# Optimization experiments

Measured on AMD Instinct MI355X. Metric: run time of the kernel, lower is better.

The kernel has to match this reference:

```python
import jax, jax.numpy as jnp
import numpy as np

N_NODES = 50000
N_EDGES = 500000
NEG_SLOPE = 0.2


def gat_layer(x, src, dst, W, a_src, a_dst, b, n):
    """PyG-style GATConv (add_self_loops=True, concat=True, eval mode).
    x: [N, F_in], W: [F_in, H*C], a_src/a_dst: [H, C], b: [H*C]."""
    H, C = a_src.shape
    h = (x @ W).reshape(-1, H, C)              # [N, H, C]
    loops = jnp.arange(n, dtype=src.dtype)
    s = jnp.concatenate([src, loops])          # self-loops appended
    d = jnp.concatenate([dst, loops])
    alpha_src = jnp.einsum('nhc,hc->nh', h, a_src)   # [N, H]
    alpha_dst = jnp.einsum('nhc,hc->nh', h, a_dst)
    e = jax.nn.leaky_relu(alpha_src[s] + alpha_dst[d], NEG_SLOPE)  # [E+N, H]
    m = jax.ops.segment_max(e, d, num_segments=n)    # segment softmax over dst
    w = jnp.exp(e - m[d])
    denom = jax.ops.segment_sum(w, d, num_segments=n)
    attn = w / (denom[d] + 1e-16)                    # [E+N, H]
    msg = h[s] * attn[:, :, None]                    # [E+N, H, C]
    out = jax.ops.segment_sum(msg, d, num_segments=n)  # [N, H, C]
    return out.reshape(n, H * C) + b


def setup_inputs() -> dict:
    key = jax.random.key(0)
    ks = jax.random.split(key, 20)
    F_in, Hd, Hh = 128, 64, 4
    g = lambda k, shp, fan: jax.random.normal(k, shp, jnp.float32) * (1.0 / np.sqrt(fan))
    inp = {
        'x': jax.random.normal(ks[0], (N_NODES, F_in), jnp.float32),
        'edge_index': jax.random.randint(ks[1], (2, N_EDGES), 0, N_NODES, jnp.int32),
        'W1': g(ks[2], (F_in, Hh * Hd), F_in),
        'a1s': g(ks[3], (Hh, Hd), Hd), 'a1d': g(ks[4], (Hh, Hd), Hd),
        'b1': jnp.zeros((Hh * Hd,), jnp.float32),
        'W2': g(ks[5], (Hh * Hd, Hh * Hd), Hh * Hd),
        'a2s': g(ks[6], (Hh, Hd), Hd), 'a2d': g(ks[7], (Hh, Hd), Hd),
        'b2': jnp.zeros((Hh * Hd,), jnp.float32),
        'W3': g(ks[8], (Hh * Hd, Hd), Hh * Hd),
        'a3s': g(ks[9], (1, Hd), Hd), 'a3d': g(ks[10], (1, Hd), Hd),
        'b3': jnp.zeros((Hd,), jnp.float32),
        'cW1': g(ks[11], (Hd, Hd // 2), Hd), 'cb1': jnp.zeros((Hd // 2,), jnp.float32),
        'cW2': g(ks[12], (Hd // 2, 2), Hd // 2), 'cb2': jnp.zeros((2,), jnp.float32),
    }
    return inp


def reference(x, edge_index, W1, a1s, a1d, b1, W2, a2s, a2d, b2,
              W3, a3s, a3d, b3, cW1, cb1, cW2, cb2):
    n = x.shape[0]
    src, dst = edge_index[0], edge_index[1]
    h = jax.nn.elu(gat_layer(x, src, dst, W1, a1s, a1d, b1, n))
    h = jax.nn.elu(gat_layer(h, src, dst, W2, a2s, a2d, b2, n))
    h = jax.nn.relu(gat_layer(h, src, dst, W3, a3s, a3d, b3, n))
    h = jax.nn.relu(h @ cW1 + cb1)
    logits = h @ cW2 + cb2
    return jax.nn.log_softmax(logits, axis=1)
```

## Files before the change

### kernel.cpp

```cpp
#include <hip/hip_runtime.h>
#include <hip/hip_fp16.h>

#define LRELU(v) ((v) > 0.f ? (v) : 0.2f * (v))
#define LOG2E 1.44269504088896340736f

typedef _Float16 f16x8 __attribute__((ext_vector_type(8)));
typedef _Float16 f16x4 __attribute__((ext_vector_type(4)));
typedef float f32x4 __attribute__((ext_vector_type(4)));

__device__ __forceinline__ float fexp2(float x) {
    return __builtin_amdgcn_exp2f(x);
}

__device__ __forceinline__ f16x8 f16x8_zero() {
    f16x8 v;
#pragma unroll
    for (int j = 0; j < 8; ++j) v[j] = (_Float16)0.f;
    return v;
}

__global__ __launch_bounds__(256) void hist_kernel(const int* __restrict__ dst,
                                                   int* __restrict__ cnt, int E) {
    int e = blockIdx.x * 256 + threadIdx.x;
    if (e < E) atomicAdd(&cnt[dst[e]], 1);
}

__global__ __launch_bounds__(256) void scan_blk(const int* __restrict__ cnt,
                                                int* __restrict__ offv,
                                                int* __restrict__ bsum, int N) {
    __shared__ int sh[256];
    const int t = threadIdx.x;
    const int base = blockIdx.x * 1024 + t * 4;
    int v0 = (base + 0 < N) ? cnt[base + 0] : 0;
    int v1 = (base + 1 < N) ? cnt[base + 1] : 0;
    int v2 = (base + 2 < N) ? cnt[base + 2] : 0;
    int v3 = (base + 3 < N) ? cnt[base + 3] : 0;
    const int T = v0 + v1 + v2 + v3;
    sh[t] = T;
    __syncthreads();
    for (int o = 1; o < 256; o <<= 1) {
        int x = (t >= o) ? sh[t - o] : 0;
        __syncthreads();
        sh[t] += x;
        __syncthreads();
    }
    const int excl = sh[t] - T;
    if (t == 255) bsum[blockIdx.x] = sh[255];
    if (base + 0 < N) offv[base + 0] = excl;
    if (base + 1 < N) offv[base + 1] = excl + v0;
    if (base + 2 < N) offv[base + 2] = excl + v0 + v1;
    if (base + 3 < N) offv[base + 3] = excl + v0 + v1 + v2;
}

__global__ __launch_bounds__(64) void scan_top(int* __restrict__ bsum,
                                               int* __restrict__ offv,
                                               int NB, int N) {
    const int t = threadIdx.x;
    const int v = (t < NB) ? bsum[t] : 0;
    int incl = v;
#pragma unroll
    for (int o = 1; o < 64; o <<= 1) {
        int x = __shfl_up(incl, o);
        if (t >= o) incl += x;
    }
    if (t < NB) bsum[t] = incl - v;
    if (t == NB - 1) offv[N] = incl;
}

__global__ __launch_bounds__(256) void scan_add(int* __restrict__ offv,
                                                const int* __restrict__ bsum, int N) {
    const int base = blockIdx.x * 1024 + threadIdx.x * 4;
    const int add = bsum[blockIdx.x];
#pragma unroll
    for (int i = 0; i < 4; ++i)
        if (base + i < N) offv[base + i] += add;
}

__global__ __launch_bounds__(256) void fill_kernel(const int* __restrict__ dst,
                                                   const int* __restrict__ srcv,
                                                   const int* __restrict__ offv,
                                                   int* __restrict__ cur,
                                                   int* __restrict__ csrsrc, int E) {
    int e = blockIdx.x * 256 + threadIdx.x;
    if (e < E) {
        int d = dst[e];
        int p = atomicAdd(&cur[d], 1);
        csrsrc[offv[d] + p] = srcv[e];
    }
}

__global__ __launch_bounds__(256) void prep_w_all(
    const float* __restrict__ W1, const float* __restrict__ W2,
    const float* __restrict__ W3, _Float16* __restrict__ Wt1,
    _Float16* __restrict__ Wt2, _Float16* __restrict__ Wt3) {
    const int S1 = 128 * 256, S2 = 256 * 256, S3 = 256 * 64;
    int idx = blockIdx.x * 256 + threadIdx.x;
    if (idx < S1) {
        int k = idx >> 8, nn = idx & 255;
        Wt1[nn * 128 + k] = (_Float16)W1[idx];
    } else if (idx < S1 + S2) {
        int i = idx - S1;
        int k = i >> 8, nn = i & 255;
        Wt2[nn * 256 + k] = (_Float16)W2[idx - S1];
    } else if (idx < S1 + S2 + S3) {
        int i = idx - S1 - S2;
        int k = i >> 6, nn = i & 63;
        Wt3[nn * 256 + k] = (_Float16)W3[i];
    }
}

template <int WM, int WN, int K, int H, bool AF32>
__global__ __launch_bounds__(WM * WN * 64) void gemm_f16_fused(
    const void* __restrict__ Av, const _Float16* __restrict__ Wt,
    const float* __restrict__ a_s, const float* __restrict__ a_d,
    _Float16* __restrict__ hout, float* __restrict__ als,
    float* __restrict__ ald, int M, int Nn) {
    constexpr int BM = WM * 64;
    constexpr int T = WM * WN * 64;
    constexpr int CHUNKS = BM * 16;
    __shared__ f16x8 Atile[BM * 16];
    const _Float16* A16 = (const _Float16*)Av;
    const float* A32 = (const float*)Av;
    const int t = threadIdx.x;
    const int lane = t & 63;
    const int wv = t >> 6;
    const int wm = wv / WN, wn = wv % WN;
    const int m0 = blockIdx.x * BM;
    const int n0 = blockIdx.y * (WN * 64);
    const int l15 = lane & 15, lg = lane >> 4;

    f32x4 acc[4][4];
    const f32x4 zz = {0.f, 0.f, 0.f, 0.f};
#pragma unroll
    for (int mi = 0; mi < 4; ++mi)
#pragma unroll
        for (int ni = 0; ni < 4; ++ni) acc[mi][ni] = zz;

    for (int kc = 0; kc < K; kc += 128) {
        __syncthreads();
#pragma unroll
        for (int i = 0; i < CHUNKS / T; ++i) {
            const int c = i * T + t;
            const int row = c >> 4, cc = c & 15;
            const int gr = m0 + row;
            f16x8 v;
            if (gr < M) {
                if constexpr (AF32) {
                    float4 p = *(const float4*)(A32 + (size_t)gr * K + kc + cc * 8);
                    float4 q = *(const float4*)(A32 + (size_t)gr * K + kc + cc * 8 + 4);
                    v[0] = (_Float16)p.x; v[1] = (_Float16)p.y;
                    v[2] = (_Float16)p.z; v[3] = (_Float16)p.w;
                    v[4] = (_Float16)q.x; v[5] = (_Float16)q.y;
                    v[6] = (_Float16)q.z; v[7] = (_Float16)q.w;
                } else {
                    v = *(const f16x8*)(A16 + (size_t)gr * K + kc + cc * 8);
                }
            } else {
                v = f16x8_zero();
            }
            Atile[(row * 16 + cc) ^ (row & 7)] = v;
        }
        __syncthreads();
#pragma unroll
        for (int ks = 0; ks < 4; ++ks) {
            f16x8 af[4], bf[4];
#pragma unroll
            for (int mi = 0; mi < 4; ++mi) {
                const int row = wm * 64 + mi * 16 + l15;
                af[mi] = Atile[(row * 16 + ks * 4 + lg) ^ (row & 7)];
            }
#pragma unroll
            for (int ni = 0; ni < 4; ++ni) {
                const int col = n0 + wn * 64 + ni * 16 + l15;
                bf[ni] = *(const f16x8*)(Wt + (size_t)col * K + kc + ks * 32 + lg * 8);
            }
#pragma unroll
            for (int mi = 0; mi < 4; ++mi)
#pragma unroll
                for (int ni = 0; ni < 4; ++ni)
                    acc[mi][ni] = __builtin_amdgcn_mfma_f32_16x16x32_f16(
                        af[mi], bf[ni], acc[mi][ni], 0, 0, 0);
        }
    }
    const int head = (n0 + wn * 64) >> 6;
    float a4s[4], a4d[4];
#pragma unroll
    for (int ni = 0; ni < 4; ++ni) {
        a4s[ni] = a_s[head * 64 + ni * 16 + l15] * LOG2E;
        a4d[ni] = a_d[head * 64 + ni * 16 + l15] * LOG2E;
    }
#pragma unroll
    for (int mi = 0; mi < 4; ++mi)
#pragma unroll
        for (int j = 0; j < 4; ++j) {
            const int r = m0 + wm * 64 + mi * 16 + lg * 4 + j;
            if (r < M) {
                float s1 = 0.f, s2 = 0.f;
#pragma unroll
                for (int ni = 0; ni < 4; ++ni) {
                    const float v = acc[mi][ni][j];
                    s1 += v * a4s[ni];
                    s2 += v * a4d[ni];
                    hout[(size_t)r * Nn + n0 + wn * 64 + ni * 16 + l15] = (_Float16)v;
                }
#pragma unroll
                for (int o = 8; o; o >>= 1) {
                    s1 += __shfl_xor(s1, o);
                    s2 += __shfl_xor(s2, o);
                }
                if (l15 == 0) {
                    als[(size_t)r * H + head] = s1;
                    ald[(size_t)r * H + head] = s2;
                }
            }
        }
}

__global__ __launch_bounds__(256) void gat_agg_h4(
    const _Float16* __restrict__ hhf, const float4* __restrict__ als4,
    const float4* __restrict__ ald4, const int* __restrict__ csrsrc,
    const int* __restrict__ offv, const float* __restrict__ bias,
    _Float16* __restrict__ outh, int N) {
    __shared__ int sidAll[4][2][36];
    __shared__ float wTAll[4][2][4][36];
    const int wv = threadIdx.x >> 6;
    const int l = threadIdx.x & 63;
    const int half = l >> 5;
    const int q = l & 31;
    const int n = (blockIdx.x * 4 + wv) * 2 + half;
    if (n >= N) return;
    const int hh = q >> 3;
    int* sid = sidAll[wv][half];
    float* wrow = wTAll[wv][half][hh];
    float (*wT)[36] = wTAll[wv][half];
    const int start = offv[n];
    const int deg = offv[n + 1] - start;
    const float4 ad = ald4[n];
    const float4 asf = als4[n];
    float4 ws4;
    ws4.x = fexp2(LRELU(asf.x + ad.x));
    ws4.y = fexp2(LRELU(asf.y + ad.y));
    ws4.z = fexp2(LRELU(asf.z + ad.z));
    ws4.w = fexp2(LRELU(asf.w + ad.w));
    float wself = ws4.x;
    wself = (hh == 1) ? ws4.y : wself;
    wself = (hh == 2) ? ws4.z : wself;
    wself = (hh == 3) ? ws4.w : wself;
    float accA[8], accB[8] = {};
    {
        const f16x8 hv = *(const f16x8*)(hhf + (size_t)n * 256 + q * 8);
#pragma unroll
        for (int c = 0; c < 8; ++c) accA[c] = (float)hv[c] * wself;
    }
    float dsum = wself;

    for (int base = 0; base < deg; base += 32) {
        const int nb = min(32, deg - base);
        int s = 0;
        float4 w4 = {0.f, 0.f, 0.f, 0.f};
        if (q < nb) {
            s = csrsrc[start + base + q];
            const float4 av = als4[s];
            w4.x = fexp2(LRELU(av.x + ad.x));
            w4.y = fexp2(LRELU(av.y + ad.y));
            w4.z = fexp2(LRELU(av.z + ad.z));
            w4.w = fexp2(LRELU(av.w + ad.w));
        }
        sid[q] = s;
        wT[0][q] = w4.x;
        wT[1][q] = w4.y;
        wT[2][q] = w4.z;
        wT[3][q] = w4.w;
        __threadfence_block();
        int i = 0;
        for (; i + 1 < nb; i += 2) {
            const int sA = sid[i], sB = sid[i + 1];
            const float wA = wrow[i], wB = wrow[i + 1];
            const f16x8 hA = *(const f16x8*)(hhf + (size_t)sA * 256 + q * 8);
            const f16x8 hB = *(const f16x8*)(hhf + (size_t)sB * 256 + q * 8);
            dsum += wA + wB;
#pragma unroll
            for (int c = 0; c < 8; ++c) {
                accA[c] += (float)hA[c] * wA;
                accB[c] += (float)hB[c] * wB;
            }
        }
        if (i < nb) {
            const int sA = sid[i];
            const float wA = wrow[i];
            const f16x8 hA = *(const f16x8*)(hhf + (size_t)sA * 256 + q * 8);
            dsum += wA;
#pragma unroll
            for (int c = 0; c < 8; ++c) accA[c] += (float)hA[c] * wA;
        }
        __threadfence_block();
    }
    const float inv = 1.f / (dsum + 1e-16f);
    const float4 bv0 = *(const float4*)(bias + q * 8);
    const float4 bv1 = *(const float4*)(bias + q * 8 + 4);
    float o8[8];
#pragma unroll
    for (int c = 0; c < 8; ++c) o8[c] = (accA[c] + accB[c]) * inv;
    o8[0] += bv0.x; o8[1] += bv0.y; o8[2] += bv0.z; o8[3] += bv0.w;
    o8[4] += bv1.x; o8[5] += bv1.y; o8[6] += bv1.z; o8[7] += bv1.w;
#pragma unroll
    for (int c = 0; c < 8; ++c)
        o8[c] = (o8[c] > 0.f) ? o8[c] : (__expf(o8[c]) - 1.f);
    f16x8 st;
#pragma unroll
    for (int c = 0; c < 8; ++c) st[c] = (_Float16)o8[c];
    *(f16x8*)(outh + (size_t)n * 256 + q * 8) = st;
}

__global__ __launch_bounds__(256) void gat_agg_h1_cls(
    const _Float16* __restrict__ hhf, const float* __restrict__ als,
    const float* __restrict__ ald, const int* __restrict__ csrsrc,
    const int* __restrict__ offv, const float* __restrict__ bias,
    const float* __restrict__ cW1, const float* __restrict__ cb1,
    const float* __restrict__ cW2, const float* __restrict__ cb2,
    float* __restrict__ outp, int N) {
    __shared__ float w1s[2048];
    __shared__ float w2s[64];
    __shared__ int sidAll[4][64];
    __shared__ float wAll[4][64];
    __shared__ float xsAll[4][64];
    for (int i = threadIdx.x; i < 2048; i += 256) w1s[i] = cW1[i];
    if (threadIdx.x < 64) w2s[threadIdx.x] = cW2[threadIdx.x];
    __syncthreads();
    const int wv = threadIdx.x >> 6;
    const int t = threadIdx.x & 63;
    const int n = blockIdx.x * 4 + wv;
    if (n >= N) return;
    int* sid = sidAll[wv];
    float* wsh = wAll[wv];
    float* xs = xsAll[wv];
    const int start = offv[n];
    const int deg = offv[n + 1] - start;
    const float ad = ald[n];
    const float wself = fexp2(LRELU(als[n] + ad));
    float a0 = (float)hhf[(size_t)n * 64 + t] * wself;
    float a1 = 0.f, a2 = 0.f, a3 = 0.f;
    float wacc = (t == 0) ? wself : 0.f;

    for (int base = 0; base < deg; base += 64) {
        const int nb = min(64, deg - base);
        int s = 0;
        float w = 0.f;
        if (t < nb) {
            s = csrsrc[start + base + t];
            w = fexp2(LRELU(als[s] + ad));
            wacc += w;
        }
        sid[t] = s;
        wsh[t] = w;
        __threadfence_block();
        int i = 0;
        for (; i + 3 < nb; i += 4) {
            const int4 ss = *(const int4*)&sid[i];
            const float4 ww = *(const float4*)&wsh[i];
            a0 += (float)hhf[(size_t)ss.x * 64 + t] * ww.x;
            a1 += (float)hhf[(size_t)ss.y * 64 + t] * ww.y;
            a2 += (float)hhf[(size_t)ss.z * 64 + t] * ww.z;
            a3 += (float)hhf[(size_t)ss.w * 64 + t] * ww.w;
        }
        for (; i < nb; ++i) {
            a0 += (float)hhf[(size_t)sid[i] * 64 + t] * wsh[i];
        }
        __threadfence_block();
    }
#pragma unroll
    for (int o = 32; o; o >>= 1) wacc += __shfl_xor(wacc, o);
    const float val = fmaxf((a0 + a1 + a2 + a3) / (wacc + 1e-16f) + bias[t], 0.f);
    xs[t] = val;
    __threadfence_block();
    const int j = t & 31;
    const int half = t >> 5;
    float s1 = 0.f;
#pragma unroll
    for (int cc = 0; cc < 32; ++cc) {
        const int c = half * 32 + cc;
        s1 += xs[c] * w1s[c * 32 + j];
    }
    s1 += __shfl_xor(s1, 32);
    const float hid = fmaxf(s1 + cb1[j], 0.f);
    const int k = t & 1, jj = t >> 1;
    const float hjj = __shfl(hid, jj);
    float s2 = hjj * w2s[jj * 2 + k];
#pragma unroll
    for (int o = 2; o < 64; o <<= 1) s2 += __shfl_xor(s2, o);
    s2 += cb2[k];
    const float a = __shfl(s2, 0);
    const float b = __shfl(s2, 1);
    const float mm = fmaxf(a, b);
    const float lse = mm + logf(__expf(a - mm) + __expf(b - mm));
    if (t < 2) outp[(size_t)n * 2 + t] = s2 - lse;
}

extern "C" void kernel_launch(void* const* d_in, const int* in_sizes, int n_in,
                              void* d_out, int out_size, void* d_ws, size_t ws_size,
                              hipStream_t stream) {
    const float* x   = (const float*)d_in[0];
    const int*   ei  = (const int*)d_in[1];
    const float* W1  = (const float*)d_in[2];
    const float* a1s = (const float*)d_in[3];
    const float* a1d = (const float*)d_in[4];
    const float* b1  = (const float*)d_in[5];
    const float* W2  = (const float*)d_in[6];
    const float* a2s = (const float*)d_in[7];
    const float* a2d = (const float*)d_in[8];
    const float* b2  = (const float*)d_in[9];
    const float* W3  = (const float*)d_in[10];
    const float* a3s = (const float*)d_in[11];
    const float* a3d = (const float*)d_in[12];
    const float* b3  = (const float*)d_in[13];
    const float* cW1 = (const float*)d_in[14];
    const float* cb1 = (const float*)d_in[15];
    const float* cW2 = (const float*)d_in[16];
    const float* cb2 = (const float*)d_in[17];

    const int N = in_sizes[0] / 128;
    const int E = in_sizes[1] / 2;
    const int* srcv = ei;
    const int* dstv = ei + E;

    char* p = (char*)d_ws;
    _Float16* slotA = (_Float16*)p; p += (size_t)N * 256 * 2;
    _Float16* slotB = (_Float16*)p; p += (size_t)N * 256 * 2;
    float* als = (float*)p; p += (size_t)N * 4 * 4;
    float* ald = (float*)p; p += (size_t)N * 4 * 4;
    int* cnt = (int*)p; p += (size_t)N * 4;
    int* offv = (int*)p; p += (size_t)(N + 4) * 4;
    int* csr = (int*)p; p += (size_t)E * 4;
    _Float16* Wt1 = (_Float16*)p; p += (size_t)128 * 256 * 2;
    _Float16* Wt2 = (_Float16*)p; p += (size_t)256 * 256 * 2;
    _Float16* Wt3 = (_Float16*)p; p += (size_t)256 * 64 * 2;
    int* bsum = (int*)p;

    prep_w_all<<<(128 * 256 + 256 * 256 + 256 * 64 + 255) / 256, 256, 0, stream>>>(
        W1, W2, W3, Wt1, Wt2, Wt3);

    const int NB = (N + 1023) / 1024;
    hipMemsetAsync(cnt, 0, (size_t)N * sizeof(int), stream);
    hist_kernel<<<(E + 255) / 256, 256, 0, stream>>>(dstv, cnt, E);
    scan_blk<<<NB, 256, 0, stream>>>(cnt, offv, bsum, N);
    scan_top<<<1, 64, 0, stream>>>(bsum, offv, NB, N);
    scan_add<<<NB, 256, 0, stream>>>(offv, bsum, N);
    hipMemsetAsync(cnt, 0, (size_t)N * sizeof(int), stream);
    fill_kernel<<<(E + 255) / 256, 256, 0, stream>>>(dstv, srcv, offv, cnt, csr, E);

    const int MB128 = (N + 127) / 128;
    const int MB256 = (N + 255) / 256;
    const int AGG8 = (N + 7) / 8;
    const int AGG4 = (N + 3) / 4;

    gemm_f16_fused<2, 4, 128, 4, true><<<dim3(MB128, 1), 512, 0, stream>>>(
        x, Wt1, a1s, a1d, slotA, als, ald, N, 256);
    gat_agg_h4<<<AGG8, 256, 0, stream>>>(slotA, (const float4*)als,
                                         (const float4*)ald, csr, offv, b1,
                                         slotB, N);

    gemm_f16_fused<2, 4, 256, 4, false><<<dim3(MB128, 1), 512, 0, stream>>>(
        slotB, Wt2, a2s, a2d, slotA, als, ald, N, 256);
    gat_agg_h4<<<AGG8, 256, 0, stream>>>(slotA, (const float4*)als,
                                         (const float4*)ald, csr, offv, b2,
                                         slotB, N);

    gemm_f16_fused<4, 1, 256, 1, false><<<dim3(MB256, 1), 256, 0, stream>>>(
        slotB, Wt3, a3s, a3d, slotA, als, ald, N, 64);
    gat_agg_h1_cls<<<AGG4, 256, 0, stream>>>(slotA, als, ald, csr,
                                             offv, b3, cW1, cb1, cW2, cb2,
                                             (float*)d_out, N);
}
```

Baseline: 272.4 us.

## Add 64-row double-buffered GEMM and split layer-3 aggregation from classifier

Layers 1 and 2 now use a new GEMM kernel with 64-row tiles, a double-buffered swizzled LDS A tile, and B fragments read straight from global memory, launching more blocks. The layer-3 aggregation now handles two nodes per wavefront with half-wave lanes each covering two channels, and writes fp16 output. A separate per-thread classifier kernel then applies the MLP and log-softmax. This aims to raise occupancy and parallelism, at the cost of an extra launch and an fp16 round-trip of the layer-3 output. It also fixes a W2 indexing expression that was equivalent in value.

```diff
diff --git a/kernel.cpp b/kernel.cpp
--- a/kernel.cpp
+++ b/kernel.cpp
@@ -6,6 +6,7 @@
 
 typedef _Float16 f16x8 __attribute__((ext_vector_type(8)));
 typedef _Float16 f16x4 __attribute__((ext_vector_type(4)));
+typedef _Float16 f16x2 __attribute__((ext_vector_type(2)));
 typedef float f32x4 __attribute__((ext_vector_type(4)));
 
 __device__ __forceinline__ float fexp2(float x) {
@@ -101,12 +102,125 @@
     } else if (idx < S1 + S2) {
         int i = idx - S1;
         int k = i >> 8, nn = i & 255;
-        Wt2[nn * 256 + k] = (_Float16)W2[idx - S1];
+        Wt2[nn * 256 + k] = (_Float16)W2[i];
     } else if (idx < S1 + S2 + S3) {
         int i = idx - S1 - S2;
         int k = i >> 6, nn = i & 63;
         Wt3[nn * 256 + k] = (_Float16)W3[i];
     }
+}
+
+template <int K, bool AF32>
+__global__ __launch_bounds__(256) void gemm64_fused(
+    const void* __restrict__ Av, const _Float16* __restrict__ Wt,
+    const float* __restrict__ a_s, const float* __restrict__ a_d,
+    _Float16* __restrict__ hout, float* __restrict__ als,
+    float* __restrict__ ald, int M) {
+    constexpr int NKC = K / 64;
+    __shared__ f16x8 Atile[2][512];
+    const _Float16* A16 = (const _Float16*)Av;
+    const float* A32 = (const float*)Av;
+    const int t = threadIdx.x;
+    const int lane = t & 63;
+    const int wn = t >> 6;
+    const int m0 = blockIdx.x * 64;
+    const int l15 = lane & 15, lg = lane >> 4;
+
+    const int r0 = t >> 3, c0 = t & 7;
+    const int r1 = (t + 256) >> 3, c1 = t & 7;
+    const int gr0 = min(m0 + r0, M - 1);
+    const int gr1 = min(m0 + r1, M - 1);
+
+    f16x8 s0, s1;
+    auto FETCH = [&](int kc) {
+        if constexpr (AF32) {
+            float4 p = *(const float4*)(A32 + (size_t)gr0 * K + kc + c0 * 8);
+            float4 q = *(const float4*)(A32 + (size_t)gr0 * K + kc + c0 * 8 + 4);
+            s0[0] = (_Float16)p.x; s0[1] = (_Float16)p.y;
+            s0[2] = (_Float16)p.z; s0[3] = (_Float16)p.w;
+            s0[4] = (_Float16)q.x; s0[5] = (_Float16)q.y;
+            s0[6] = (_Float16)q.z; s0[7] = (_Float16)q.w;
+            float4 r = *(const float4*)(A32 + (size_t)gr1 * K + kc + c1 * 8);
+            float4 u = *(const float4*)(A32 + (size_t)gr1 * K + kc + c1 * 8 + 4);
+            s1[0] = (_Float16)r.x; s1[1] = (_Float16)r.y;
+            s1[2] = (_Float16)r.z; s1[3] = (_Float16)r.w;
+            s1[4] = (_Float16)u.x; s1[5] = (_Float16)u.y;
+            s1[6] = (_Float16)u.z; s1[7] = (_Float16)u.w;
+        } else {
+            s0 = *(const f16x8*)(A16 + (size_t)gr0 * K + kc + c0 * 8);
+            s1 = *(const f16x8*)(A16 + (size_t)gr1 * K + kc + c1 * 8);
+        }
+    };
+    FETCH(0);
+
+    f32x4 acc[4][4];
+    const f32x4 zz = {0.f, 0.f, 0.f, 0.f};
+#pragma unroll
+    for (int mi = 0; mi < 4; ++mi)
+#pragma unroll
+        for (int ni = 0; ni < 4; ++ni) acc[mi][ni] = zz;
+
+    int cur = 0;
+#pragma unroll
+    for (int kci = 0; kci < NKC; ++kci) {
+        Atile[cur][r0 * 8 + (c0 ^ (r0 & 7))] = s0;
+        Atile[cur][r1 * 8 + (c1 ^ (r1 & 7))] = s1;
+        __syncthreads();
+        if (kci + 1 < NKC) FETCH((kci + 1) * 64);
+#pragma unroll
+        for (int ks = 0; ks < 2; ++ks) {
+            f16x8 af[4], bf[4];
+#pragma unroll
+            for (int mi = 0; mi < 4; ++mi) {
+                const int row = mi * 16 + l15;
+                af[mi] = Atile[cur][row * 8 + ((ks * 4 + lg) ^ (row & 7))];
+            }
+#pragma unroll
+            for (int ni = 0; ni < 4; ++ni) {
+                const int col = wn * 64 + ni * 16 + l15;
+                bf[ni] = *(const f16x8*)(Wt + (size_t)col * K + kci * 64 + ks * 32 + lg * 8);
+            }
+#pragma unroll
+            for (int mi = 0; mi < 4; ++mi)
+#pragma unroll
+                for (int ni = 0; ni < 4; ++ni)
+                    acc[mi][ni] = __builtin_amdgcn_mfma_f32_16x16x32_f16(
+                        af[mi], bf[ni], acc[mi][ni], 0, 0, 0);
+        }
+        cur ^= 1;
+    }
+    const int head = wn;
+    float a4s[4], a4d[4];
+#pragma unroll
+    for (int ni = 0; ni < 4; ++ni) {
+        a4s[ni] = a_s[head * 64 + ni * 16 + l15] * LOG2E;
+        a4d[ni] = a_d[head * 64 + ni * 16 + l15] * LOG2E;
+    }
+#pragma unroll
+    for (int mi = 0; mi < 4; ++mi)
+#pragma unroll
+        for (int j = 0; j < 4; ++j) {
+            const int r = m0 + mi * 16 + lg * 4 + j;
+            if (r < M) {
+                float s1v = 0.f, s2v = 0.f;
+#pragma unroll
+                for (int ni = 0; ni < 4; ++ni) {
+                    const float v = acc[mi][ni][j];
+                    s1v += v * a4s[ni];
+                    s2v += v * a4d[ni];
+                    hout[(size_t)r * 256 + wn * 64 + ni * 16 + l15] = (_Float16)v;
+                }
+#pragma unroll
+                for (int o = 8; o; o >>= 1) {
+                    s1v += __shfl_xor(s1v, o);
+                    s2v += __shfl_xor(s2v, o);
+                }
+                if (l15 == 0) {
+                    als[(size_t)r * 4 + head] = s1v;
+                    ald[(size_t)r * 4 + head] = s2v;
+                }
+            }
+        }
 }
 
 template <int WM, int WN, int K, int H, bool AF32>
@@ -312,88 +426,96 @@
     *(f16x8*)(outh + (size_t)n * 256 + q * 8) = st;
 }
 
-__global__ __launch_bounds__(256) void gat_agg_h1_cls(
+__global__ __launch_bounds__(256) void gat_agg_h1(
     const _Float16* __restrict__ hhf, const float* __restrict__ als,
     const float* __restrict__ ald, const int* __restrict__ csrsrc,
     const int* __restrict__ offv, const float* __restrict__ bias,
-    const float* __restrict__ cW1, const float* __restrict__ cb1,
-    const float* __restrict__ cW2, const float* __restrict__ cb2,
-    float* __restrict__ outp, int N) {
-    __shared__ float w1s[2048];
-    __shared__ float w2s[64];
-    __shared__ int sidAll[4][64];
-    __shared__ float wAll[4][64];
-    __shared__ float xsAll[4][64];
-    for (int i = threadIdx.x; i < 2048; i += 256) w1s[i] = cW1[i];
-    if (threadIdx.x < 64) w2s[threadIdx.x] = cW2[threadIdx.x];
-    __syncthreads();
+    _Float16* __restrict__ outh, int N) {
+    __shared__ int sidAll[4][2][36];
+    __shared__ float wAll[4][2][36];
     const int wv = threadIdx.x >> 6;
-    const int t = threadIdx.x & 63;
-    const int n = blockIdx.x * 4 + wv;
+    const int l = threadIdx.x & 63;
+    const int half = l >> 5;
+    const int q = l & 31;
+    const int n = (blockIdx.x * 4 + wv) * 2 + half;
     if (n >= N) return;
-    int* sid = sidAll[wv];
-    float* wsh = wAll[wv];
-    float* xs = xsAll[wv];
+    int* sid = sidAll[wv][half];
+    float* wsh = wAll[wv][half];
     const int start = offv[n];
     const int deg = offv[n + 1] - start;
     const float ad = ald[n];
     const float wself = fexp2(LRELU(als[n] + ad));
-    float a0 = (float)hhf[(size_t)n * 64 + t] * wself;
-    float a1 = 0.f, a2 = 0.f, a3 = 0.f;
-    float wacc = (t == 0) ? wself : 0.f;
-
-    for (int base = 0; base < deg; base += 64) {
-        const int nb = min(64, deg - base);
+    float acc0, acc1;
+    {
+        const f16x2 hv = *(const f16x2*)(hhf + (size_t)n * 64 + q * 2);
+        acc0 = (float)hv[0] * wself;
+        acc1 = (float)hv[1] * wself;
+    }
+    float dsum = wself;
+
+    for (int base = 0; base < deg; base += 32) {
+        const int nb = min(32, deg - base);
         int s = 0;
         float w = 0.f;
-        if (t < nb) {
-            s = csrsrc[start + base + t];
+        if (q < nb) {
+            s = csrsrc[start + base + q];
             w = fexp2(LRELU(als[s] + ad));
-            wacc += w;
-        }
-        sid[t] = s;
-        wsh[t] = w;
+        }
+        sid[q] = s;
+        wsh[q] = w;
         __threadfence_block();
-        int i = 0;
-        for (; i + 3 < nb; i += 4) {
-            const int4 ss = *(const int4*)&sid[i];
-            const float4 ww = *(const float4*)&wsh[i];
-            a0 += (float)hhf[(size_t)ss.x * 64 + t] * ww.x;
-            a1 += (float)hhf[(size_t)ss.y * 64 + t] * ww.y;
-            a2 += (float)hhf[(size_t)ss.z * 64 + t] * ww.z;
-            a3 += (float)hhf[(size_t)ss.w * 64 + t] * ww.w;
-        }
-        for (; i < nb; ++i) {
-            a0 += (float)hhf[(size_t)sid[i] * 64 + t] * wsh[i];
+        for (int i = 0; i < nb; ++i) {
+            const int si = sid[i];
+            const float wi = wsh[i];
+            const f16x2 hv = *(const f16x2*)(hhf + (size_t)si * 64 + q * 2);
+            dsum += wi;
+            acc0 += (float)hv[0] * wi;
+            acc1 += (float)hv[1] * wi;
         }
         __threadfence_block();
     }
-#pragma unroll
-    for (int o = 32; o; o >>= 1) wacc += __shfl_xor(wacc, o);
-    const float val = fmaxf((a0 + a1 + a2 + a3) / (wacc + 1e-16f) + bias[t], 0.f);
-    xs[t] = val;
-    __threadfence_block();
-    const int j = t & 31;
-    const int half = t >> 5;
-    float s1 = 0.f;
-#pragma unroll
-    for (int cc = 0; cc < 32; ++cc) {
-        const int c = half * 32 + cc;
-        s1 += xs[c] * w1s[c * 32 + j];
-    }
-    s1 += __shfl_xor(s1, 32);
-    const float hid = fmaxf(s1 + cb1[j], 0.f);
-    const int k = t & 1, jj = t >> 1;
-    const float hjj = __shfl(hid, jj);
-    float s2 = hjj * w2s[jj * 2 + k];
-#pragma unroll
-    for (int o = 2; o < 64; o <<= 1) s2 += __shfl_xor(s2, o);
-    s2 += cb2[k];
-    const float a = __shfl(s2, 0);
-    const float b = __shfl(s2, 1);
-    const float mm = fmaxf(a, b);
-    const float lse = mm + logf(__expf(a - mm) + __expf(b - mm));
-    if (t < 2) outp[(size_t)n * 2 + t] = s2 - lse;
+    const float inv = 1.f / (dsum + 1e-16f);
+    const float v0 = fmaxf(acc0 * inv + bias[q * 2], 0.f);
+    const float v1 = fmaxf(acc1 * inv + bias[q * 2 + 1], 0.f);
+    f16x2 st;
+    st[0] = (_Float16)v0;
+    st[1] = (_Float16)v1;
+    *(f16x2*)(outh + (size_t)n * 64 + q * 2) = st;
+}
+
+__global__ __launch_bounds__(256) void classifier_ls(
+    const _Float16* __restrict__ h3, const float* __restrict__ cW1,
+    const float* __restrict__ cb1, const float* __restrict__ cW2,
+    const float* __restrict__ cb2, float* __restrict__ outp, int N) {
+    __shared__ float w1s[2048];
+    __shared__ float w2s[64];
+    __shared__ float b1s[32];
+    for (int i = threadIdx.x; i < 2048; i += 256) w1s[i] = cW1[i];
+    if (threadIdx.x < 64) w2s[threadIdx.x] = cW2[threadIdx.x];
+    if (threadIdx.x < 32) b1s[threadIdx.x] = cb1[threadIdx.x];
+    __syncthreads();
+    const int n = blockIdx.x * 256 + threadIdx.x;
+    if (n >= N) return;
+    float x[64];
+#pragma unroll
+    for (int i = 0; i < 8; ++i) {
+        const f16x8 v = *(const f16x8*)(h3 + (size_t)n * 64 + i * 8);
+#pragma unroll
+        for (int j = 0; j < 8; ++j) x[i * 8 + j] = (float)v[j];
+    }
+    float l0 = cb2[0], l1 = cb2[1];
+    for (int j = 0; j < 32; ++j) {
+        float s = b1s[j];
+#pragma unroll
+        for (int c = 0; c < 64; ++c) s += x[c] * w1s[c * 32 + j];
+        s = fmaxf(s, 0.f);
+        l0 += s * w2s[j * 2];
+        l1 += s * w2s[j * 2 + 1];
+    }
+    const float mm = fmaxf(l0, l1);
+    const float lse = mm + logf(__expf(l0 - mm) + __expf(l1 - mm));
+    outp[(size_t)n * 2 + 0] = l0 - lse;
+    outp[(size_t)n * 2 + 1] = l1 - lse;
 }
 
 extern "C" void kernel_launch(void* const* d_in, const int* in_sizes, int n_in,
@@ -448,26 +570,28 @@
     hipMemsetAsync(cnt, 0, (size_t)N * sizeof(int), stream);
     fill_kernel<<<(E + 255) / 256, 256, 0, stream>>>(dstv, srcv, offv, cnt, csr, E);
 
-    const int MB128 = (N + 127) / 128;
+    const int MB64 = (N + 63) / 64;
     const int MB256 = (N + 255) / 256;
     const int AGG8 = (N + 7) / 8;
-    const int AGG4 = (N + 3) / 4;
-
-    gemm_f16_fused<2, 4, 128, 4, true><<<dim3(MB128, 1), 512, 0, stream>>>(
-        x, Wt1, a1s, a1d, slotA, als, ald, N, 256);
+    const int CLS = (N + 255) / 256;
+
+    gemm64_fused<128, true><<<MB64, 256, 0, stream>>>(
+        x, Wt1, a1s, a1d, slotA, als, ald, N);
     gat_agg_h4<<<AGG8, 256, 0, stream>>>(slotA, (const float4*)als,
                                          (const float4*)ald, csr, offv, b1,
                                          slotB, N);
 
-    gemm_f16_fused<2, 4, 256, 4, false><<<dim3(MB128, 1), 512, 0, stream>>>(
-        slotB, Wt2, a2s, a2d, slotA, als, ald, N, 256);
+    gemm64_fused<256, false><<<MB64, 256, 0, stream>>>(
+        slotB, Wt2, a2s, a2d, slotA, als, ald, N);
     gat_agg_h4<<<AGG8, 256, 0, stream>>>(slotA, (const float4*)als,
                                          (const float4*)ald, csr, offv, b2,
                                          slotB, N);
 
     gemm_f16_fused<4, 1, 256, 1, false><<<dim3(MB256, 1), 256, 0, stream>>>(
         slotB, Wt3, a3s, a3d, slotA, als, ald, N, 64);
-    gat_agg_h1_cls<<<AGG4, 256, 0, stream>>>(slotA, als, ald, csr,
-                                             offv, b3, cW1, cb1, cW2, cb2,
-                                             (float*)d_out, N);
-}
+    gat_agg_h1<<<AGG8, 256, 0, stream>>>(slotA, als, ald, csr, offv, b3,
+                                         slotB, N);
+
+    classifier_ls<<<CLS, 256, 0, stream>>>(slotB, cW1, cb1, cW2, cb2,
+                                           (float*)d_out, N);
+}
```

Measured after the change: 276.1 us. No clear change (+1.4%).
